# Optimization experiments

Measured on AMD Instinct MI355X. Metric: run time of the kernel, lower is better.

Reference implementation:

```python
import jax, jax.numpy as jnp
import numpy as np

HH = 38  # sqrt(amd0=1444)
KD = 3   # 3x3 neighborhood


def setup_inputs() -> dict:
    key = jax.random.key(0)
    fm = jax.random.normal(key, (16, 512, HH, HH), dtype=jnp.float32)
    return {"fm": fm}


def reference(fm):
    # fm: [B, C, H, W] -> replication pad 1 -> NHWC -> gather 3x3 neighbors,
    # concatenated along the channel axis in row-major neighbor order
    # (matching counts[:, 0..8] = (h-1,w-1),(h-1,w),(h-1,w+1),(h,w-1),...).
    B, C, H, W = fm.shape
    x = jnp.pad(fm, ((0, 0), (0, 0), (1, 1), (1, 1)), mode="edge")  # [B,C,H+2,W+2]
    x = jnp.transpose(x, (0, 2, 3, 1))  # [B, H+2, W+2, C]
    patches = [x[:, di:di + H, dj:dj + W, :] for di in range(KD) for dj in range(KD)]
    pfm = jnp.concatenate(patches, axis=-1)  # [B, H, W, 9*C]
    return pfm.reshape(B, H * W, KD * KD * C)  # [B, 1444, 9*C]
```

## Files before the change

### kernel.cpp

```cpp
#include <hip/hip_runtime.h>


#define BB 16
#define CC 512
#define HH 38
#define WW 38
#define HW (HH * WW)
#define KK 9
#define NT 512

template <int HALF>
__device__ __forceinline__ void do_half(const float* __restrict__ fm,
                                        float* __restrict__ out,
                                        int b, int hp, int c)
{
    constexpr int W0 = HALF * 19;
    constexpr int WN = 19;
    constexpr int WA = HALF * 18;
    constexpr int NL = 10;

    const int r0 = (hp > 0) ? hp - 1 : 0;
    const int r2 = (hp < HH - 1) ? hp + 1 : HH - 1;
    const int rows[3] = { r0, hp, r2 };

    const float* plane = fm + (size_t)(b * CC + c) * HW;

    float v[3][2 * NL];
    #pragma unroll
    for (int di = 0; di < 3; ++di) {
        const float2* src = (const float2*)(plane + rows[di] * WW + WA);
        #pragma unroll
        for (int i = 0; i < NL; ++i) {
            const float2 t = src[i];
            v[di][2 * i + 0] = t.x;
            v[di][2 * i + 1] = t.y;
        }
    }

    float* outp = out + (size_t)((b * HW + hp * WW + W0) * KK) * CC + c;
    #pragma unroll
    for (int wi = 0; wi < WN; ++wi) {
        #pragma unroll
        for (int di = 0; di < 3; ++di) {
            #pragma unroll
            for (int dj = 0; dj < 3; ++dj) {
                int wj = W0 + wi + dj - 1;
                wj = wj < 0 ? 0 : (wj > WW - 1 ? WW - 1 : wj);
                __builtin_nontemporal_store(
                    v[di][wj - WA],
                    outp + (size_t)(wi * KK + di * 3 + dj) * CC);
            }
        }
    }
}

__global__ __launch_bounds__(NT) void spatial_pool_gather(
    const float* __restrict__ fm, float* __restrict__ out)
{
    const unsigned L = blockIdx.x;
    const int xcd  = (int)(L & 7u);
    const int slot = (int)(L >> 3);
    const int bsel = slot / 76;
    const int rem  = slot - bsel * 76;
    const int hp   = rem >> 1;
    const int half = rem & 1;
    const int b    = xcd + 8 * bsel;
    const int c    = (int)threadIdx.x;

    if (half == 0) do_half<0>(fm, out, b, hp, c);
    else           do_half<1>(fm, out, b, hp, c);
}

extern "C" void kernel_launch(void* const* d_in, const int* in_sizes, int n_in,
                              void* d_out, int out_size, void* d_ws, size_t ws_size,
                              hipStream_t stream) {
    const float* fm = (const float*)d_in[0];
    float* out = (float*)d_out;
    dim3 grid(BB * HH * 2);
    dim3 block(NT);
    spatial_pool_gather<<<grid, block, 0, stream>>>(fm, out);
}
```

Baseline: 463.2 us.

## Vectorize output stores to 4 channels per thread and split width into eighths

Each thread now handles four consecutive channels and writes 16-byte nontemporal vector stores instead of scalar stores. The width is split into eight sub-ranges, with each block covering two of them, and the grid grows to four blocks per row with 256 threads each. The aim is fewer store instructions and wider write transactions on this write-bound gather. In exchange, loads come from four separate channel planes per thread and are less coalesced, and more input is re-read because of the overlapping halo columns.

```diff
diff --git a/kernel.cpp b/kernel.cpp
--- a/kernel.cpp
+++ b/kernel.cpp
@@ -7,37 +7,41 @@
 #define WW 38
 #define HW (HH * WW)
 #define KK 9
-#define NT 512
+#define NT 256
 
-template <int HALF>
-__device__ __forceinline__ void do_half(const float* __restrict__ fm,
-                                        float* __restrict__ out,
-                                        int b, int hp, int c)
+typedef float f32x2 __attribute__((ext_vector_type(2)));
+typedef float f32x4 __attribute__((ext_vector_type(4)));
+
+template <int W0, int WN, int WA, int NL>
+__device__ __forceinline__ void do_sub(const float* __restrict__ fm,
+                                       float* __restrict__ out,
+                                       int b, int hp, int c0)
 {
-    constexpr int W0 = HALF * 19;
-    constexpr int WN = 19;
-    constexpr int WA = HALF * 18;
-    constexpr int NL = 10;
-
     const int r0 = (hp > 0) ? hp - 1 : 0;
     const int r2 = (hp < HH - 1) ? hp + 1 : HH - 1;
     const int rows[3] = { r0, hp, r2 };
 
-    const float* plane = fm + (size_t)(b * CC + c) * HW;
+    const float* p0 = fm + (size_t)(b * CC + c0 + 0) * HW;
+    const float* p1 = fm + (size_t)(b * CC + c0 + 1) * HW;
+    const float* p2 = fm + (size_t)(b * CC + c0 + 2) * HW;
+    const float* p3 = fm + (size_t)(b * CC + c0 + 3) * HW;
 
-    float v[3][2 * NL];
+    f32x4 vv[3][2 * NL];
     #pragma unroll
     for (int di = 0; di < 3; ++di) {
-        const float2* src = (const float2*)(plane + rows[di] * WW + WA);
+        const int ro = rows[di] * WW + WA;
         #pragma unroll
         for (int i = 0; i < NL; ++i) {
-            const float2 t = src[i];
-            v[di][2 * i + 0] = t.x;
-            v[di][2 * i + 1] = t.y;
+            const f32x2 t0 = *(const f32x2*)(p0 + ro + 2 * i);
+            const f32x2 t1 = *(const f32x2*)(p1 + ro + 2 * i);
+            const f32x2 t2 = *(const f32x2*)(p2 + ro + 2 * i);
+            const f32x2 t3 = *(const f32x2*)(p3 + ro + 2 * i);
+            vv[di][2 * i + 0] = (f32x4){t0.x, t1.x, t2.x, t3.x};
+            vv[di][2 * i + 1] = (f32x4){t0.y, t1.y, t2.y, t3.y};
         }
     }
 
-    float* outp = out + (size_t)((b * HW + hp * WW + W0) * KK) * CC + c;
+    float* outp = out + (size_t)((b * HW + hp * WW + W0) * KK) * CC + c0;
     #pragma unroll
     for (int wi = 0; wi < WN; ++wi) {
         #pragma unroll
@@ -47,28 +51,41 @@
                 int wj = W0 + wi + dj - 1;
                 wj = wj < 0 ? 0 : (wj > WW - 1 ? WW - 1 : wj);
                 __builtin_nontemporal_store(
-                    v[di][wj - WA],
-                    outp + (size_t)(wi * KK + di * 3 + dj) * CC);
+                    vv[di][wj - WA],
+                    (f32x4*)(outp + (size_t)(wi * KK + di * 3 + dj) * CC));
             }
         }
     }
 }
 
-__global__ __launch_bounds__(NT) void spatial_pool_gather(
+__global__ __launch_bounds__(NT) void spatial_pool_x4(
     const float* __restrict__ fm, float* __restrict__ out)
 {
     const unsigned L = blockIdx.x;
     const int xcd  = (int)(L & 7u);
     const int slot = (int)(L >> 3);
-    const int bsel = slot / 76;
-    const int rem  = slot - bsel * 76;
-    const int hp   = rem >> 1;
-    const int half = rem & 1;
+    const int bsel = slot / 152;
+    const int rem  = slot - bsel * 152;
+    const int hp   = rem >> 2;
+    const int qq   = rem & 3;
     const int b    = xcd + 8 * bsel;
-    const int c    = (int)threadIdx.x;
 
-    if (half == 0) do_half<0>(fm, out, b, hp, c);
-    else           do_half<1>(fm, out, b, hp, c);
+    const int tid = (int)threadIdx.x;
+    const int cg  = tid & 127;
+    const int sub = tid >> 7;
+    const int c0  = 4 * cg;
+    const int ws  = qq * 2 + sub;
+
+    switch (ws) {
+        case 0:  do_sub< 0, 5,  0, 3>(fm, out, b, hp, c0); break;
+        case 1:  do_sub< 5, 5,  4, 4>(fm, out, b, hp, c0); break;
+        case 2:  do_sub<10, 5,  8, 4>(fm, out, b, hp, c0); break;
+        case 3:  do_sub<15, 4, 14, 3>(fm, out, b, hp, c0); break;
+        case 4:  do_sub<19, 5, 18, 4>(fm, out, b, hp, c0); break;
+        case 5:  do_sub<24, 5, 22, 4>(fm, out, b, hp, c0); break;
+        case 6:  do_sub<29, 5, 28, 4>(fm, out, b, hp, c0); break;
+        default: do_sub<34, 4, 32, 3>(fm, out, b, hp, c0); break;
+    }
 }
 
 extern "C" void kernel_launch(void* const* d_in, const int* in_sizes, int n_in,
@@ -76,7 +93,7 @@
                               hipStream_t stream) {
     const float* fm = (const float*)d_in[0];
     float* out = (float*)d_out;
-    dim3 grid(BB * HH * 2);
+    dim3 grid(BB * HH * 4);
     dim3 block(NT);
-    spatial_pool_gather<<<grid, block, 0, stream>>>(fm, out);
+    spatial_pool_x4<<<grid, block, 0, stream>>>(fm, out);
 }
```

Result: no change. 454.4 us (-1.9%).
